# Optimization experiments

Hardware: AMD Instinct MI355X
Metric: run time of the kernel (lower is better)

Reference implementation:

```python
import jax, jax.numpy as jnp
import numpy as np

N = 8192   # number of points (p) == number of reference points (r); must match for final bmm
D = 1024   # feature width of the Linear projections


def setup_inputs() -> dict:
    key = jax.random.key(0)
    ks = jax.random.split(key, 8)
    s = 1.0 / np.sqrt(D)
    return {
        "p": jax.random.normal(ks[0], (N, D), dtype=jnp.float32),
        "r": jax.random.normal(ks[1], (N, D), dtype=jnp.float32),
        "Wh": jax.random.uniform(ks[2], (D, D), jnp.float32, -s, s),
        "bh": jax.random.uniform(ks[3], (D,), jnp.float32, -s, s),
        "Wl": jax.random.uniform(ks[4], (D, D), jnp.float32, -s, s),
        "bl": jax.random.uniform(ks[5], (D,), jnp.float32, -s, s),
        "Wg": jax.random.uniform(ks[6], (D, D), jnp.float32, -s, s),
        "bg": jax.random.uniform(ks[7], (D,), jnp.float32, -s, s),
    }


def reference(p, r, Wh, bh, Wl, bl, Wg, bg):
    # Linear projections (torch Linear: x @ W.T + b)
    q = p @ Wh.T + bh          # [N, D]  M_h(p)
    k = r @ Wl.T + bl          # [N, D]  M_l(r)
    v = p @ Wg.T + bg          # [N, D]  M_g(p)
    scores = q @ k.T           # [N, N]  == bmm(q[None], k[None].transpose(1,2))[0]
    # torch softmax dim=1 on [1, N, N] normalizes over the QUERY axis -> axis=0 here
    attn = jax.nn.softmax(scores, axis=0)
    return p + attn @ v        # residual add
```

## Files before the change

kernel.cpp:

```cpp
#include <hip/hip_runtime.h>
#include <hip/hip_fp16.h>

typedef _Float16 f16;
typedef __attribute__((ext_vector_type(8))) _Float16 f16x8;
typedef __attribute__((ext_vector_type(4))) float f32x4;

#define NPTS 8192
#define DIM  1024
#define HL2E 0.721347520444482f
#define S2SHIFT 50.0f
#define TBUF (128 * 32)

__device__ __forceinline__ void glds16(const void* g, void* l) {
  __builtin_amdgcn_global_load_lds(
      (const __attribute__((address_space(1))) void*)g,
      (__attribute__((address_space(3))) void*)l, 16, 0, 0);
}


__global__ void cvt_f32_f16(const float* __restrict__ src, f16* __restrict__ dst, int n) {
  int i = (blockIdx.x * 256 + threadIdx.x) * 8;
  if (i >= n) return;
  const float4* s = (const float4*)(src + i);
  float4 a = s[0], b = s[1];
  f16x8 o;
  o[0] = (f16)a.x; o[1] = (f16)a.y; o[2] = (f16)a.z; o[3] = (f16)a.w;
  o[4] = (f16)b.x; o[5] = (f16)b.y; o[6] = (f16)b.z; o[7] = (f16)b.w;
  *(f16x8*)(dst + i) = o;
}

__global__ void zero_f32(float* __restrict__ p, int n) {
  int i = blockIdx.x * 256 + threadIdx.x;
  if (i < n) p[i] = 0.f;
}

__global__ void mk_scales(const float* __restrict__ colsum,
                          f16* __restrict__ ics2, f16* __restrict__ ics4) {
  int j = blockIdx.x * 256 + threadIdx.x;
  float r2 = rsqrtf(fmaxf(colsum[j], 1e-20f));
  ics2[j] = (f16)r2;
  ics4[j] = (f16)sqrtf(r2);
}

__global__ void vscale(f16* __restrict__ vt, const f16* __restrict__ ics2) {
  long i = ((long)blockIdx.x * 256 + threadIdx.x) * 8;
  f16x8 v = *(f16x8*)(vt + i);
  f16x8 s = *(const f16x8*)(ics2 + (i & (NPTS - 1)));
  *(f16x8*)(vt + i) = v * s;
}

__global__ void reduce_out(const float* __restrict__ p,
                           const float* __restrict__ pa,
                           const float* __restrict__ pb,
                           float* __restrict__ out) {
  long i = ((long)blockIdx.x * 256 + threadIdx.x) * 4;
  float4 a = *(const float4*)(p + i);
  float4 b = *(const float4*)(pa + i);
  float4 c = *(const float4*)(pb + i);
  a.x += b.x + c.x; a.y += b.y + c.y; a.z += b.z + c.z; a.w += b.w + c.w;
  *(float4*)(out + i) = a;
}

__global__ __launch_bounds__(256, 2)
void proj_fused(const f16* __restrict__ p_h, const f16* __restrict__ r_h,
                const f16* __restrict__ Wh, const f16* __restrict__ Wl,
                const f16* __restrict__ Wg,
                const float* __restrict__ bh, const float* __restrict__ bl,
                const float* __restrict__ bg,
                f16* __restrict__ q_h, f16* __restrict__ k_h,
                f16* __restrict__ vt_h) {
  __shared__ f16 sA[2 * TBUF];
  __shared__ f16 sB[2 * TBUF];
  const int sub = blockIdx.x >> 9;
  const int bl_ = blockIdx.x & 511;
  const long bi = (long)(bl_ & 63) * 128;
  const long bj = (long)(bl_ >> 6) * 128;
  const f16* A = (sub == 1) ? r_h : p_h;
  const f16* B = (sub == 0) ? Wh : (sub == 1) ? Wl : Wg;
  const float* bias = (sub == 0) ? bh : (sub == 1) ? bl : bg;

  const int t = threadIdx.x;
  const int w = t >> 6, l = t & 63;
  const int wm = (w >> 1) * 64, wn = (w & 1) * 64;
  const int lr = l & 15;
  const int fbase = lr * 32 + (((l >> 4) ^ ((lr >> 1) & 3)) * 8);
  const int grow = w * 16 + (l >> 2);
  const int gcol = ((l & 3) ^ ((l >> 3) & 3)) * 8;
  const f16* gA = A + (bi + grow) * (long)DIM + gcol;
  const f16* gB = B + (bj + grow) * (long)DIM + gcol;
  const int lw0 = (w * 16) * 32, lw1 = (64 + w * 16) * 32;

  glds16(gA, sA + lw0);
  glds16(gA + 64l * DIM, sA + lw1);
  glds16(gB, sB + lw0);
  glds16(gB + 64l * DIM, sB + lw1);
  gA += 32; gB += 32;

  f32x4 acc[4][4] = {};
  const int nk = DIM / 32;
  for (int k = 0; k < nk; k++) {
    const int cur = (k & 1) * TBUF, nxt = TBUF - cur;
    __syncthreads();
    if (k + 1 < nk) {
      glds16(gA, sA + nxt + lw0);
      glds16(gA + 64l * DIM, sA + nxt + lw1);
      glds16(gB, sB + nxt + lw0);
      glds16(gB + 64l * DIM, sB + nxt + lw1);
      gA += 32; gB += 32;
    }
    f16x8 af[4], bf[4];
#pragma unroll
    for (int mt = 0; mt < 4; mt++)
      af[mt] = *(const f16x8*)(sA + cur + (wm + mt * 16) * 32 + fbase);
#pragma unroll
    for (int nt = 0; nt < 4; nt++)
      bf[nt] = *(const f16x8*)(sB + cur + (wn + nt * 16) * 32 + fbase);
#pragma unroll
    for (int mt = 0; mt < 4; mt++)
#pragma unroll
      for (int nt = 0; nt < 4; nt++)
        acc[mt][nt] = __builtin_amdgcn_mfma_f32_16x16x32_f16(af[mt], bf[nt], acc[mt][nt], 0, 0, 0);
  }

  const int rbase = (l >> 4) * 4;
  f16* C = (sub == 0) ? q_h : (sub == 1) ? k_h : vt_h;
#pragma unroll
  for (int nt = 0; nt < 4; nt++) {
    const long col = bj + wn + nt * 16 + lr;
    const float bb = bias[col];
#pragma unroll
    for (int mt = 0; mt < 4; mt++) {
      const long row0 = bi + wm + mt * 16 + rbase;
      if (sub < 2) {
#pragma unroll
        for (int g = 0; g < 4; g++)
          C[(row0 + g) * DIM + col] = (f16)(acc[mt][nt][g] + bb);
      } else {
        union { unsigned long long u; f16 h[4]; } pk;
#pragma unroll
        for (int g = 0; g < 4; g++) pk.h[g] = (f16)(acc[mt][nt][g] + bb);
        *(unsigned long long*)(C + col * (long)NPTS + row0) = pk.u;
      }
    }
  }
}

__global__ __launch_bounds__(512, 2)
void gemm_qk(const f16* __restrict__ A, const f16* __restrict__ B,
             f16* __restrict__ S, float* __restrict__ colsum) {
  __shared__ f16 smem[4 * 16384];
  const int b = blockIdx.x;
  const int sx = b & 7;
  const int j = b >> 3;
  const long bi = (long)(j >> 2) * 256;
  const long bj = (long)(sx * 4 + (j & 3)) * 256;

  const int t = threadIdx.x;
  const int w = t >> 6, l = t & 63;
  const int wm = (w >> 2) * 128, wn = (w & 3) * 64;
  const int lr = l & 15;
  const int fbase = lr * 32 + (((l >> 4) ^ ((lr >> 1) & 3)) * 8);
  const int sro = t >> 2;
  const int scol = ((t & 3) ^ ((t >> 3) & 3)) * 8;
  const f16* gAs = A + (bi + sro) * (long)DIM + scol;
  const f16* gBs = B + (bj + sro) * (long)DIM + scol;
  const int ldst = w * 512;

#pragma unroll
  for (int tl = 0; tl < 3; ++tl) {
    f16* d = smem + tl * 16384;
    glds16(gAs + tl * 32,              d + ldst);
    glds16(gAs + tl * 32 + 128l * DIM, d + 4096 + ldst);
    glds16(gBs + tl * 32,              d + 8192 + ldst);
    glds16(gBs + tl * 32 + 128l * DIM, d + 12288 + ldst);
  }
  asm volatile("s_waitcnt vmcnt(8)" ::: "memory");
  __builtin_amdgcn_s_barrier();
  asm volatile("" ::: "memory");

  f32x4 acc[8][4] = {};
#pragma unroll 4
  for (int kt = 0; kt < 32; ++kt) {
    const f16* sa = smem + (kt & 3) * 16384;
    f16* d = smem + ((kt + 3) & 3) * 16384;
    const int ks = (kt + 3 < 32) ? (kt + 3) : 31;
    const f16* as_ = gAs + ks * 32;
    const f16* bs_ = gBs + ks * 32;
    f16x8 af[4], bf[4];

#pragma unroll
    for (int mt = 0; mt < 4; ++mt)
      af[mt] = *(const f16x8*)(sa + (wm + mt * 16) * 32 + fbase);
#pragma unroll
    for (int nt = 0; nt < 4; ++nt)
      bf[nt] = *(const f16x8*)(sa + 8192 + (wn + nt * 16) * 32 + fbase);
    glds16(as_,              d + ldst);
    glds16(as_ + 128l * DIM, d + 4096 + ldst);
#pragma unroll
    for (int mt = 0; mt < 4; ++mt)
#pragma unroll
      for (int nt = 0; nt < 4; ++nt)
        acc[mt][nt] = __builtin_amdgcn_mfma_f32_16x16x32_f16(af[mt], bf[nt], acc[mt][nt], 0, 0, 0);

#pragma unroll
    for (int mt = 0; mt < 4; ++mt)
      af[mt] = *(const f16x8*)(sa + (wm + 64 + mt * 16) * 32 + fbase);
    glds16(bs_,              d + 8192 + ldst);
    glds16(bs_ + 128l * DIM, d + 12288 + ldst);
#pragma unroll
    for (int mt = 0; mt < 4; ++mt)
#pragma unroll
      for (int nt = 0; nt < 4; ++nt)
        acc[4 + mt][nt] = __builtin_amdgcn_mfma_f32_16x16x32_f16(af[mt], bf[nt], acc[4 + mt][nt], 0, 0, 0);

    asm volatile("s_waitcnt vmcnt(8)" ::: "memory");
    __builtin_amdgcn_s_barrier();
    asm volatile("" ::: "memory");
  }

  const int rbase = (l >> 4) * 4;
  float csum[4] = {0.f, 0.f, 0.f, 0.f};
#pragma unroll
  for (int mt = 0; mt < 8; ++mt) {
#pragma unroll
    for (int g = 0; g < 4; ++g) {
      const long row = bi + wm + mt * 16 + rbase + g;
      f16* Srow = S + row * NPTS + bj + wn + lr;
#pragma unroll
      for (int nt = 0; nt < 4; ++nt) {
        float e = exp2f((acc[mt][nt][g] - S2SHIFT) * HL2E);
        e = fminf(e, 240.f);
        f16 eh = (f16)e;
        Srow[nt * 16] = eh;
        float ef = (float)eh;
        csum[nt] += ef * ef;
      }
    }
  }
#pragma unroll
  for (int nt = 0; nt < 4; ++nt) {
    float cs = csum[nt];
    cs += __shfl_xor(cs, 16);
    cs += __shfl_xor(cs, 32);
    if (l < 16) atomicAdd(colsum + (bj + wn + nt * 16 + lr), cs);
  }
}

__global__ __launch_bounds__(512, 2)
void gemm_pv(const f16* __restrict__ Sm, const f16* __restrict__ vt,
             const f16* __restrict__ ics4,
             float* __restrict__ part0, float* __restrict__ part1) {
  __shared__ f16 smem[4 * 16384];
  const int b = blockIdx.x;
  const int sx = b & 7;
  const int q = b >> 3;
  const int bjidx = q & 3;
  const int pr = (q >> 2) * 8 + sx;
  const int split = pr >> 5;
  const long bi = (long)(pr & 31) * 256;
  const long bj = (long)bjidx * 256;
  const long koff = (long)split * (NPTS / 2);

  const int t = threadIdx.x;
  const int w = t >> 6, l = t & 63;
  const int wm = (w >> 2) * 128, wn = (w & 3) * 64;
  const int lr = l & 15;
  const int fbase = lr * 32 + (((l >> 4) ^ ((lr >> 1) & 3)) * 8);
  const int sro = t >> 2;
  const int scol = ((t & 3) ^ ((t >> 3) & 3)) * 8;
  const f16* gAs = Sm + (bi + sro) * (long)NPTS + koff + scol;
  const f16* gBs = vt + (bj + sro) * (long)NPTS + koff + scol;
  const f16* gic = ics4 + koff + (l >> 4) * 8;
  const int ldst = w * 512;

  const int nk = (NPTS / 2) / 32;

  f16x8 icf[2];
  icf[0] = *(const f16x8*)(gic);
  icf[1] = *(const f16x8*)(gic + 32);
#pragma unroll
  for (int tl = 0; tl < 3; ++tl) {
    f16* d = smem + tl * 16384;
    glds16(gAs + tl * 32,               d + ldst);
    glds16(gAs + tl * 32 + 128l * NPTS, d + 4096 + ldst);
    glds16(gBs + tl * 32,               d + 8192 + ldst);
    glds16(gBs + tl * 32 + 128l * NPTS, d + 12288 + ldst);
  }
  asm volatile("s_waitcnt vmcnt(8)" ::: "memory");
  __builtin_amdgcn_s_barrier();
  asm volatile("" ::: "memory");

  f32x4 acc[8][4] = {};
#pragma unroll 4
  for (int kt = 0; kt < nk; ++kt) {
    const f16* sa = smem + (kt & 3) * 16384;
    f16* d = smem + ((kt + 3) & 3) * 16384;
    const int ks = (kt + 3 < nk) ? (kt + 3) : nk - 1;
    const int ki = (kt + 2 < nk) ? (kt + 2) : nk - 1;
    const f16* as_ = gAs + ks * 32;
    const f16* bs_ = gBs + ks * 32;
    f16x8 af[4], bf[4];

    const f16x8 ic_now = icf[kt & 1];
    icf[kt & 1] = *(const f16x8*)(gic + ki * 32);

#pragma unroll
    for (int mt = 0; mt < 4; ++mt) {
      af[mt] = *(const f16x8*)(sa + (wm + mt * 16) * 32 + fbase);
      af[mt] = af[mt] * ic_now;
      af[mt] = af[mt] * af[mt];
    }
#pragma unroll
    for (int nt = 0; nt < 4; ++nt)
      bf[nt] = *(const f16x8*)(sa + 8192 + (wn + nt * 16) * 32 + fbase);
    glds16(as_,               d + ldst);
    glds16(as_ + 128l * NPTS, d + 4096 + ldst);
#pragma unroll
    for (int mt = 0; mt < 4; ++mt)
#pragma unroll
      for (int nt = 0; nt < 4; ++nt)
        acc[mt][nt] = __builtin_amdgcn_mfma_f32_16x16x32_f16(af[mt], bf[nt], acc[mt][nt], 0, 0, 0);

#pragma unroll
    for (int mt = 0; mt < 4; ++mt) {
      af[mt] = *(const f16x8*)(sa + (wm + 64 + mt * 16) * 32 + fbase);
      af[mt] = af[mt] * ic_now;
      af[mt] = af[mt] * af[mt];
    }
    glds16(bs_,               d + 8192 + ldst);
    glds16(bs_ + 128l * NPTS, d + 12288 + ldst);
#pragma unroll
    for (int mt = 0; mt < 4; ++mt)
#pragma unroll
      for (int nt = 0; nt < 4; ++nt)
        acc[4 + mt][nt] = __builtin_amdgcn_mfma_f32_16x16x32_f16(af[mt], bf[nt], acc[4 + mt][nt], 0, 0, 0);

    asm volatile("s_waitcnt vmcnt(10)" ::: "memory");
    __builtin_amdgcn_s_barrier();
    asm volatile("" ::: "memory");
  }

  float* part = split ? part1 : part0;
  const int rbase = (l >> 4) * 4;
#pragma unroll
  for (int mt = 0; mt < 8; ++mt) {
#pragma unroll
    for (int g = 0; g < 4; ++g) {
      const long row = bi + wm + mt * 16 + rbase + g;
      float* Prow = part + row * DIM + bj + wn + lr;
#pragma unroll
      for (int nt = 0; nt < 4; ++nt)
        Prow[nt * 16] = acc[mt][nt][g];
    }
  }
}

extern "C" void kernel_launch(void* const* d_in, const int* in_sizes, int n_in,
                              void* d_out, int out_size, void* d_ws, size_t ws_size,
                              hipStream_t stream) {
  const float* p  = (const float*)d_in[0];
  const float* r  = (const float*)d_in[1];
  const float* Wh = (const float*)d_in[2];
  const float* bh = (const float*)d_in[3];
  const float* Wl = (const float*)d_in[4];
  const float* bl = (const float*)d_in[5];
  const float* Wg = (const float*)d_in[6];
  const float* bg = (const float*)d_in[7];
  float* out = (float*)d_out;

  char* ws = (char*)d_ws;
  f16* q_h  = (f16*)(ws + (0ull  << 20));
  f16* k_h  = (f16*)(ws + (16ull << 20));
  f16* vt_h = (f16*)(ws + (32ull << 20));
  f16* p_h  = (f16*)(ws + (48ull << 20));
  f16* r_h  = (f16*)(ws + (64ull << 20));
  f16* wh_h = (f16*)(ws + (80ull << 20));
  f16* wl_h = (f16*)(ws + (82ull << 20));
  f16* wg_h = (f16*)(ws + (84ull << 20));
  f16* S    = (f16*)(ws + (96ull << 20));
  float* colsum = (float*)(ws + (224ull << 20));
  f16* ics2 = (f16*)(ws + (225ull << 20));
  f16* ics4 = (f16*)(ws + (226ull << 20));
  float* part0 = (float*)(ws + (0ull  << 20));
  float* part1 = (float*)(ws + (48ull << 20));

  const int nP = NPTS * DIM, nW = DIM * DIM;
  cvt_f32_f16<<<nP / 2048, 256, 0, stream>>>(p,  p_h,  nP);
  cvt_f32_f16<<<nP / 2048, 256, 0, stream>>>(r,  r_h,  nP);
  cvt_f32_f16<<<nW / 2048, 256, 0, stream>>>(Wh, wh_h, nW);
  cvt_f32_f16<<<nW / 2048, 256, 0, stream>>>(Wl, wl_h, nW);
  cvt_f32_f16<<<nW / 2048, 256, 0, stream>>>(Wg, wg_h, nW);
  zero_f32<<<NPTS / 256, 256, 0, stream>>>(colsum, NPTS);

  dim3 blk(256);
  proj_fused<<<1536, blk, 0, stream>>>(p_h, r_h, wh_h, wl_h, wg_h,
                                       bh, bl, bg, q_h, k_h, vt_h);
  gemm_qk<<<1024, dim3(512), 0, stream>>>(q_h, k_h, S, colsum);
  mk_scales<<<NPTS / 256, 256, 0, stream>>>(colsum, ics2, ics4);
  vscale<<<(NPTS / 8) * (DIM / 256), 256, 0, stream>>>(vt_h, ics2);
  gemm_pv<<<256, dim3(512), 0, stream>>>(S, vt_h, ics4, part0, part1);
  reduce_out<<<nP / 1024, 256, 0, stream>>>(p, part0, part1, out);
}
```

Measured before the change: 501.4 us.

## Shrink GEMM tiles to 256x128 with 3-stage LDS ring for higher occupancy

```diff
diff --git a/kernel.cpp b/kernel.cpp
--- a/kernel.cpp
+++ b/kernel.cpp
@@ -9,7 +9,7 @@
 #define DIM  1024
 #define HL2E 0.721347520444482f
 #define S2SHIFT 50.0f
-#define TBUF (128 * 32)
+#define BUF3 12288
 
 __device__ __forceinline__ void glds16(const void* g, void* l) {
   __builtin_amdgcn_global_load_lds(
@@ -61,7 +61,7 @@
   *(float4*)(out + i) = a;
 }
 
-__global__ __launch_bounds__(256, 2)
+__global__ __launch_bounds__(512, 4)
 void proj_fused(const f16* __restrict__ p_h, const f16* __restrict__ r_h,
                 const f16* __restrict__ Wh, const f16* __restrict__ Wl,
                 const f16* __restrict__ Wg,
@@ -69,12 +69,12 @@
                 const float* __restrict__ bg,
                 f16* __restrict__ q_h, f16* __restrict__ k_h,
                 f16* __restrict__ vt_h) {
-  __shared__ f16 sA[2 * TBUF];
-  __shared__ f16 sB[2 * TBUF];
-  const int sub = blockIdx.x >> 9;
-  const int bl_ = blockIdx.x & 511;
-  const long bi = (long)(bl_ & 63) * 128;
-  const long bj = (long)(bl_ >> 6) * 128;
+  __shared__ f16 smem[3 * BUF3];
+  const int b = blockIdx.x;
+  const int sub = b >> 8;
+  const int rest = b & 255;
+  const long bj = (long)(rest & 7) * 128;
+  const long bi = (long)(rest >> 3) * 256;
   const f16* A = (sub == 1) ? r_h : p_h;
   const f16* B = (sub == 0) ? Wh : (sub == 1) ? Wl : Wg;
   const float* bias = (sub == 0) ? bh : (sub == 1) ? bl : bg;
@@ -82,82 +82,6 @@
   const int t = threadIdx.x;
   const int w = t >> 6, l = t & 63;
   const int wm = (w >> 1) * 64, wn = (w & 1) * 64;
-  const int lr = l & 15;
-  const int fbase = lr * 32 + (((l >> 4) ^ ((lr >> 1) & 3)) * 8);
-  const int grow = w * 16 + (l >> 2);
-  const int gcol = ((l & 3) ^ ((l >> 3) & 3)) * 8;
-  const f16* gA = A + (bi + grow) * (long)DIM + gcol;
-  const f16* gB = B + (bj + grow) * (long)DIM + gcol;
-  const int lw0 = (w * 16) * 32, lw1 = (64 + w * 16) * 32;
-
-  glds16(gA, sA + lw0);
-  glds16(gA + 64l * DIM, sA + lw1);
-  glds16(gB, sB + lw0);
-  glds16(gB + 64l * DIM, sB + lw1);
-  gA += 32; gB += 32;
-
-  f32x4 acc[4][4] = {};
-  const int nk = DIM / 32;
-  for (int k = 0; k < nk; k++) {
-    const int cur = (k & 1) * TBUF, nxt = TBUF - cur;
-    __syncthreads();
-    if (k + 1 < nk) {
-      glds16(gA, sA + nxt + lw0);
-      glds16(gA + 64l * DIM, sA + nxt + lw1);
-      glds16(gB, sB + nxt + lw0);
-      glds16(gB + 64l * DIM, sB + nxt + lw1);
-      gA += 32; gB += 32;
-    }
-    f16x8 af[4], bf[4];
-#pragma unroll
-    for (int mt = 0; mt < 4; mt++)
-      af[mt] = *(const f16x8*)(sA + cur + (wm + mt * 16) * 32 + fbase);
-#pragma unroll
-    for (int nt = 0; nt < 4; nt++)
-      bf[nt] = *(const f16x8*)(sB + cur + (wn + nt * 16) * 32 + fbase);
-#pragma unroll
-    for (int mt = 0; mt < 4; mt++)
-#pragma unroll
-      for (int nt = 0; nt < 4; nt++)
-        acc[mt][nt] = __builtin_amdgcn_mfma_f32_16x16x32_f16(af[mt], bf[nt], acc[mt][nt], 0, 0, 0);
-  }
-
-  const int rbase = (l >> 4) * 4;
-  f16* C = (sub == 0) ? q_h : (sub == 1) ? k_h : vt_h;
-#pragma unroll
-  for (int nt = 0; nt < 4; nt++) {
-    const long col = bj + wn + nt * 16 + lr;
-    const float bb = bias[col];
-#pragma unroll
-    for (int mt = 0; mt < 4; mt++) {
-      const long row0 = bi + wm + mt * 16 + rbase;
-      if (sub < 2) {
-#pragma unroll
-        for (int g = 0; g < 4; g++)
-          C[(row0 + g) * DIM + col] = (f16)(acc[mt][nt][g] + bb);
-      } else {
-        union { unsigned long long u; f16 h[4]; } pk;
-#pragma unroll
-        for (int g = 0; g < 4; g++) pk.h[g] = (f16)(acc[mt][nt][g] + bb);
-        *(unsigned long long*)(C + col * (long)NPTS + row0) = pk.u;
-      }
-    }
-  }
-}
-
-__global__ __launch_bounds__(512, 2)
-void gemm_qk(const f16* __restrict__ A, const f16* __restrict__ B,
-             f16* __restrict__ S, float* __restrict__ colsum) {
-  __shared__ f16 smem[4 * 16384];
-  const int b = blockIdx.x;
-  const int sx = b & 7;
-  const int j = b >> 3;
-  const long bi = (long)(j >> 2) * 256;
-  const long bj = (long)(sx * 4 + (j & 3)) * 256;
-
-  const int t = threadIdx.x;
-  const int w = t >> 6, l = t & 63;
-  const int wm = (w >> 2) * 128, wn = (w & 3) * 64;
   const int lr = l & 15;
   const int fbase = lr * 32 + (((l >> 4) ^ ((lr >> 1) & 3)) * 8);
   const int sro = t >> 2;
@@ -167,61 +91,133 @@
   const int ldst = w * 512;
 
 #pragma unroll
-  for (int tl = 0; tl < 3; ++tl) {
-    f16* d = smem + tl * 16384;
+  for (int tl = 0; tl < 2; ++tl) {
+    f16* d = smem + tl * BUF3;
     glds16(gAs + tl * 32,              d + ldst);
     glds16(gAs + tl * 32 + 128l * DIM, d + 4096 + ldst);
     glds16(gBs + tl * 32,              d + 8192 + ldst);
-    glds16(gBs + tl * 32 + 128l * DIM, d + 12288 + ldst);
-  }
-  asm volatile("s_waitcnt vmcnt(8)" ::: "memory");
+  }
+  asm volatile("s_waitcnt vmcnt(3)" ::: "memory");
   __builtin_amdgcn_s_barrier();
   asm volatile("" ::: "memory");
 
-  f32x4 acc[8][4] = {};
-#pragma unroll 4
-  for (int kt = 0; kt < 32; ++kt) {
-    const f16* sa = smem + (kt & 3) * 16384;
-    f16* d = smem + ((kt + 3) & 3) * 16384;
-    const int ks = (kt + 3 < 32) ? (kt + 3) : 31;
-    const f16* as_ = gAs + ks * 32;
-    const f16* bs_ = gBs + ks * 32;
+  f32x4 acc[4][4] = {};
+  const int nk = DIM / 32;
+  int cOff = 0, tOff = 2 * BUF3;
+  for (int kt = 0; kt < nk; ++kt) {
+    const f16* sa = smem + cOff;
+    f16* d = smem + tOff;
+    const int ks = (kt + 2 < nk) ? (kt + 2) : nk - 1;
     f16x8 af[4], bf[4];
-
 #pragma unroll
     for (int mt = 0; mt < 4; ++mt)
       af[mt] = *(const f16x8*)(sa + (wm + mt * 16) * 32 + fbase);
 #pragma unroll
     for (int nt = 0; nt < 4; ++nt)
       bf[nt] = *(const f16x8*)(sa + 8192 + (wn + nt * 16) * 32 + fbase);
-    glds16(as_,              d + ldst);
-    glds16(as_ + 128l * DIM, d + 4096 + ldst);
+    glds16(gAs + ks * 32,              d + ldst);
+    glds16(gAs + ks * 32 + 128l * DIM, d + 4096 + ldst);
+    glds16(gBs + ks * 32,              d + 8192 + ldst);
 #pragma unroll
     for (int mt = 0; mt < 4; ++mt)
 #pragma unroll
       for (int nt = 0; nt < 4; ++nt)
         acc[mt][nt] = __builtin_amdgcn_mfma_f32_16x16x32_f16(af[mt], bf[nt], acc[mt][nt], 0, 0, 0);
-
-#pragma unroll
-    for (int mt = 0; mt < 4; ++mt)
-      af[mt] = *(const f16x8*)(sa + (wm + 64 + mt * 16) * 32 + fbase);
-    glds16(bs_,              d + 8192 + ldst);
-    glds16(bs_ + 128l * DIM, d + 12288 + ldst);
-#pragma unroll
-    for (int mt = 0; mt < 4; ++mt)
-#pragma unroll
-      for (int nt = 0; nt < 4; ++nt)
-        acc[4 + mt][nt] = __builtin_amdgcn_mfma_f32_16x16x32_f16(af[mt], bf[nt], acc[4 + mt][nt], 0, 0, 0);
-
-    asm volatile("s_waitcnt vmcnt(8)" ::: "memory");
+    asm volatile("s_waitcnt vmcnt(3)" ::: "memory");
     __builtin_amdgcn_s_barrier();
     asm volatile("" ::: "memory");
+    cOff += BUF3; if (cOff == 3 * BUF3) cOff = 0;
+    tOff += BUF3; if (tOff == 3 * BUF3) tOff = 0;
+  }
+
+  const int rbase = (l >> 4) * 4;
+  f16* C = (sub == 0) ? q_h : (sub == 1) ? k_h : vt_h;
+#pragma unroll
+  for (int nt = 0; nt < 4; ++nt) {
+    const long col = bj + wn + nt * 16 + lr;
+    const float bb = bias[col];
+#pragma unroll
+    for (int mt = 0; mt < 4; ++mt) {
+      const long row0 = bi + wm + mt * 16 + rbase;
+      if (sub < 2) {
+#pragma unroll
+        for (int g = 0; g < 4; ++g)
+          C[(row0 + g) * DIM + col] = (f16)(acc[mt][nt][g] + bb);
+      } else {
+        union { unsigned long long u; f16 h[4]; } pk;
+#pragma unroll
+        for (int g = 0; g < 4; ++g) pk.h[g] = (f16)(acc[mt][nt][g] + bb);
+        *(unsigned long long*)(C + col * (long)NPTS + row0) = pk.u;
+      }
+    }
+  }
+}
+
+__global__ __launch_bounds__(512, 4)
+void gemm_qk(const f16* __restrict__ A, const f16* __restrict__ B,
+             f16* __restrict__ S, float* __restrict__ colsum) {
+  __shared__ f16 smem[3 * BUF3];
+  const int b = blockIdx.x;
+  const int sx = b & 7;
+  const int j = b >> 3;
+  const long bi = (long)(j >> 3) * 256;
+  const long bj = (long)(sx * 8 + (j & 7)) * 128;
+
+  const int t = threadIdx.x;
+  const int w = t >> 6, l = t & 63;
+  const int wm = (w >> 1) * 64, wn = (w & 1) * 64;
+  const int lr = l & 15;
+  const int fbase = lr * 32 + (((l >> 4) ^ ((lr >> 1) & 3)) * 8);
+  const int sro = t >> 2;
+  const int scol = ((t & 3) ^ ((t >> 3) & 3)) * 8;
+  const f16* gAs = A + (bi + sro) * (long)DIM + scol;
+  const f16* gBs = B + (bj + sro) * (long)DIM + scol;
+  const int ldst = w * 512;
+
+#pragma unroll
+  for (int tl = 0; tl < 2; ++tl) {
+    f16* d = smem + tl * BUF3;
+    glds16(gAs + tl * 32,              d + ldst);
+    glds16(gAs + tl * 32 + 128l * DIM, d + 4096 + ldst);
+    glds16(gBs + tl * 32,              d + 8192 + ldst);
+  }
+  asm volatile("s_waitcnt vmcnt(3)" ::: "memory");
+  __builtin_amdgcn_s_barrier();
+  asm volatile("" ::: "memory");
+
+  f32x4 acc[4][4] = {};
+  const int nk = DIM / 32;
+  int cOff = 0, tOff = 2 * BUF3;
+  for (int kt = 0; kt < nk; ++kt) {
+    const f16* sa = smem + cOff;
+    f16* d = smem + tOff;
+    const int ks = (kt + 2 < nk) ? (kt + 2) : nk - 1;
+    f16x8 af[4], bf[4];
+#pragma unroll
+    for (int mt = 0; mt < 4; ++mt)
+      af[mt] = *(const f16x8*)(sa + (wm + mt * 16) * 32 + fbase);
+#pragma unroll
+    for (int nt = 0; nt < 4; ++nt)
+      bf[nt] = *(const f16x8*)(sa + 8192 + (wn + nt * 16) * 32 + fbase);
+    glds16(gAs + ks * 32,              d + ldst);
+    glds16(gAs + ks * 32 + 128l * DIM, d + 4096 + ldst);
+    glds16(gBs + ks * 32,              d + 8192 + ldst);
+#pragma unroll
+    for (int mt = 0; mt < 4; ++mt)
+#pragma unroll
+      for (int nt = 0; nt < 4; ++nt)
+        acc[mt][nt] = __builtin_amdgcn_mfma_f32_16x16x32_f16(af[mt], bf[nt], acc[mt][nt], 0, 0, 0);
+    asm volatile("s_waitcnt vmcnt(3)" ::: "memory");
+    __builtin_amdgcn_s_barrier();
+    asm volatile("" ::: "memory");
+    cOff += BUF3; if (cOff == 3 * BUF3) cOff = 0;
+    tOff += BUF3; if (tOff == 3 * BUF3) tOff = 0;
   }
 
   const int rbase = (l >> 4) * 4;
   float csum[4] = {0.f, 0.f, 0.f, 0.f};
 #pragma unroll
-  for (int mt = 0; mt < 8; ++mt) {
+  for (int mt = 0; mt < 4; ++mt) {
 #pragma unroll
     for (int g = 0; g < 4; ++g) {
       const long row = bi + wm + mt * 16 + rbase + g;
@@ -246,24 +242,23 @@
   }
 }
 
-__global__ __launch_bounds__(512, 2)
+__global__ __launch_bounds__(512, 4)
 void gemm_pv(const f16* __restrict__ Sm, const f16* __restrict__ vt,
              const f16* __restrict__ ics4,
              float* __restrict__ part0, float* __restrict__ part1) {
-  __shared__ f16 smem[4 * 16384];
+  __shared__ f16 smem[3 * BUF3];
   const int b = blockIdx.x;
   const int sx = b & 7;
   const int q = b >> 3;
-  const int bjidx = q & 3;
-  const int pr = (q >> 2) * 8 + sx;
-  const int split = pr >> 5;
-  const long bi = (long)(pr & 31) * 256;
-  const long bj = (long)bjidx * 256;
+  const int pp = sx * 2 + (q & 1);
+  const long bj = (long)(pp & 7) * 128;
+  const int split = pp >> 3;
+  const long bi = (long)(q >> 1) * 256;
   const long koff = (long)split * (NPTS / 2);
 
   const int t = threadIdx.x;
   const int w = t >> 6, l = t & 63;
-  const int wm = (w >> 2) * 128, wn = (w & 3) * 64;
+  const int wm = (w >> 1) * 64, wn = (w & 1) * 64;
   const int lr = l & 15;
   const int fbase = lr * 32 + (((l >> 4) ^ ((lr >> 1) & 3)) * 8);
   const int sro = t >> 2;
@@ -275,35 +270,29 @@
 
   const int nk = (NPTS / 2) / 32;
 
-  f16x8 icf[2];
-  icf[0] = *(const f16x8*)(gic);
-  icf[1] = *(const f16x8*)(gic + 32);
-#pragma unroll
-  for (int tl = 0; tl < 3; ++tl) {
-    f16* d = smem + tl * 16384;
+  f16x8 ic0 = *(const f16x8*)(gic);
+  f16x8 ic1 = *(const f16x8*)(gic + 32);
+#pragma unroll
+  for (int tl = 0; tl < 2; ++tl) {
+    f16* d = smem + tl * BUF3;
     glds16(gAs + tl * 32,               d + ldst);
     glds16(gAs + tl * 32 + 128l * NPTS, d + 4096 + ldst);
     glds16(gBs + tl * 32,               d + 8192 + ldst);
-    glds16(gBs + tl * 32 + 128l * NPTS, d + 12288 + ldst);
-  }
-  asm volatile("s_waitcnt vmcnt(8)" ::: "memory");
+  }
+  asm volatile("s_waitcnt vmcnt(3)" ::: "memory");
   __builtin_amdgcn_s_barrier();
   asm volatile("" ::: "memory");
 
-  f32x4 acc[8][4] = {};
-#pragma unroll 4
+  f32x4 acc[4][4] = {};
+  int cOff = 0, tOff = 2 * BUF3;
   for (int kt = 0; kt < nk; ++kt) {
-    const f16* sa = smem + (kt & 3) * 16384;
-    f16* d = smem + ((kt + 3) & 3) * 16384;
-    const int ks = (kt + 3 < nk) ? (kt + 3) : nk - 1;
-    const int ki = (kt + 2 < nk) ? (kt + 2) : nk - 1;
-    const f16* as_ = gAs + ks * 32;
-    const f16* bs_ = gBs + ks * 32;
+    const f16* sa = smem + cOff;
+    f16* d = smem + tOff;
+    const int ks = (kt + 2 < nk) ? (kt + 2) : nk - 1;
+    const f16x8 ic_now = ic0;
+    ic0 = ic1;
+    ic1 = *(const f16x8*)(gic + ks * 32);
     f16x8 af[4], bf[4];
-
-    const f16x8 ic_now = icf[kt & 1];
-    icf[kt & 1] = *(const f16x8*)(gic + ki * 32);
-
 #pragma unroll
     for (int mt = 0; mt < 4; ++mt) {
       af[mt] = *(const f16x8*)(sa + (wm + mt * 16) * 32 + fbase);
@@ -313,37 +302,25 @@
 #pragma unroll
     for (int nt = 0; nt < 4; ++nt)
       bf[nt] = *(const f16x8*)(sa + 8192 + (wn + nt * 16) * 32 + fbase);
-    glds16(as_,               d + ldst);
-    glds16(as_ + 128l * NPTS, d + 4096 + ldst);
+    glds16(gAs + ks * 32,               d + ldst);
+    glds16(gAs + ks * 32 + 128l * NPTS, d + 4096 + ldst);
+    glds16(gBs + ks * 32,               d + 8192 + ldst);
 #pragma unroll
     for (int mt = 0; mt < 4; ++mt)
 #pragma unroll
       for (int nt = 0; nt < 4; ++nt)
         acc[mt][nt] = __builtin_amdgcn_mfma_f32_16x16x32_f16(af[mt], bf[nt], acc[mt][nt], 0, 0, 0);
-
-#pragma unroll
-    for (int mt = 0; mt < 4; ++mt) {
-      af[mt] = *(const f16x8*)(sa + (wm + 64 + mt * 16) * 32 + fbase);
-      af[mt] = af[mt] * ic_now;
-      af[mt] = af[mt] * af[mt];
-    }
-    glds16(bs_,               d + 8192 + ldst);
-    glds16(bs_ + 128l * NPTS, d + 12288 + ldst);
-#pragma unroll
-    for (int mt = 0; mt < 4; ++mt)
-#pragma unroll
-      for (int nt = 0; nt < 4; ++nt)
-        acc[4 + mt][nt] = __builtin_amdgcn_mfma_f32_16x16x32_f16(af[mt], bf[nt], acc[4 + mt][nt], 0, 0, 0);
-
-    asm volatile("s_waitcnt vmcnt(10)" ::: "memory");
+    asm volatile("s_waitcnt vmcnt(4)" ::: "memory");
     __builtin_amdgcn_s_barrier();
     asm volatile("" ::: "memory");
+    cOff += BUF3; if (cOff == 3 * BUF3) cOff = 0;
+    tOff += BUF3; if (tOff == 3 * BUF3) tOff = 0;
   }
 
   float* part = split ? part1 : part0;
   const int rbase = (l >> 4) * 4;
 #pragma unroll
-  for (int mt = 0; mt < 8; ++mt) {
+  for (int mt = 0; mt < 4; ++mt) {
 #pragma unroll
     for (int g = 0; g < 4; ++g) {
       const long row = bi + wm + mt * 16 + rbase + g;
@@ -392,12 +369,11 @@
   cvt_f32_f16<<<nW / 2048, 256, 0, stream>>>(Wg, wg_h, nW);
   zero_f32<<<NPTS / 256, 256, 0, stream>>>(colsum, NPTS);
 
-  dim3 blk(256);
-  proj_fused<<<1536, blk, 0, stream>>>(p_h, r_h, wh_h, wl_h, wg_h,
-                                       bh, bl, bg, q_h, k_h, vt_h);
-  gemm_qk<<<1024, dim3(512), 0, stream>>>(q_h, k_h, S, colsum);
+  proj_fused<<<768, dim3(512), 0, stream>>>(p_h, r_h, wh_h, wl_h, wg_h,
+                                            bh, bl, bg, q_h, k_h, vt_h);
+  gemm_qk<<<2048, dim3(512), 0, stream>>>(q_h, k_h, S, colsum);
   mk_scales<<<NPTS / 256, 256, 0, stream>>>(colsum, ics2, ics4);
   vscale<<<(NPTS / 8) * (DIM / 256), 256, 0, stream>>>(vt_h, ics2);
-  gemm_pv<<<256, dim3(512), 0, stream>>>(S, vt_h, ics4, part0, part1);
+  gemm_pv<<<512, dim3(512), 0, stream>>>(S, vt_h, ics4, part0, part1);
   reduce_out<<<nP / 1024, 256, 0, stream>>>(p, part0, part1, out);
 }
```

Result: slower. 527.8 us (+5.3%).

## Prefetch next k-tile LDS fragments into registers in QK and PV GEMM loops

Applied to the files above, without the earlier changes.

```diff
diff --git a/kernel.cpp b/kernel.cpp
--- a/kernel.cpp
+++ b/kernel.cpp
@@ -145,6 +145,40 @@
   }
 }
 
+#define QK_BODY(KT, PA, PB, NA, NB)                                          \
+  {                                                                          \
+    const int kq = (KT);                                                     \
+    const f16* sa = smem + (kq & 3) * 16384;                                 \
+    const int ksn = (kq + 1 < 32) ? (kq + 1) : 31;                           \
+    const f16* sn = smem + (ksn & 3) * 16384;                                \
+    f16* d = smem + ((kq + 3) & 3) * 16384;                                  \
+    const int ks = (kq + 3 < 32) ? (kq + 3) : 31;                            \
+    const f16* as_ = gAs + ks * 32;                                          \
+    const f16* bs_ = gBs + ks * 32;                                          \
+    f16x8 af2[4];                                                            \
+    _Pragma("unroll") for (int mt = 0; mt < 4; ++mt)                         \
+      af2[mt] = *(const f16x8*)(sa + (wm + 64 + mt * 16) * 32 + fbase);      \
+    glds16(as_,              d + ldst);                                      \
+    glds16(as_ + 128l * DIM, d + 4096 + ldst);                               \
+    _Pragma("unroll") for (int mt = 0; mt < 4; ++mt)                         \
+      _Pragma("unroll") for (int nt = 0; nt < 4; ++nt)                       \
+        acc[mt][nt] = __builtin_amdgcn_mfma_f32_16x16x32_f16(                \
+            PA[mt], PB[nt], acc[mt][nt], 0, 0, 0);                           \
+    glds16(bs_,              d + 8192 + ldst);                               \
+    glds16(bs_ + 128l * DIM, d + 12288 + ldst);                              \
+    _Pragma("unroll") for (int mt = 0; mt < 4; ++mt)                         \
+      _Pragma("unroll") for (int nt = 0; nt < 4; ++nt)                       \
+        acc[4 + mt][nt] = __builtin_amdgcn_mfma_f32_16x16x32_f16(            \
+            af2[mt], PB[nt], acc[4 + mt][nt], 0, 0, 0);                      \
+    _Pragma("unroll") for (int mt = 0; mt < 4; ++mt)                         \
+      NA[mt] = *(const f16x8*)(sn + (wm + mt * 16) * 32 + fbase);            \
+    _Pragma("unroll") for (int nt = 0; nt < 4; ++nt)                         \
+      NB[nt] = *(const f16x8*)(sn + 8192 + (wn + nt * 16) * 32 + fbase);     \
+    asm volatile("s_waitcnt vmcnt(4)" ::: "memory");                         \
+    __builtin_amdgcn_s_barrier();                                            \
+    asm volatile("" ::: "memory");                                           \
+  }
+
 __global__ __launch_bounds__(512, 2)
 void gemm_qk(const f16* __restrict__ A, const f16* __restrict__ B,
              f16* __restrict__ S, float* __restrict__ colsum) {
@@ -174,48 +208,22 @@
     glds16(gBs + tl * 32,              d + 8192 + ldst);
     glds16(gBs + tl * 32 + 128l * DIM, d + 12288 + ldst);
   }
-  asm volatile("s_waitcnt vmcnt(8)" ::: "memory");
+  asm volatile("s_waitcnt vmcnt(4)" ::: "memory");
   __builtin_amdgcn_s_barrier();
   asm volatile("" ::: "memory");
 
   f32x4 acc[8][4] = {};
-#pragma unroll 4
-  for (int kt = 0; kt < 32; ++kt) {
-    const f16* sa = smem + (kt & 3) * 16384;
-    f16* d = smem + ((kt + 3) & 3) * 16384;
-    const int ks = (kt + 3 < 32) ? (kt + 3) : 31;
-    const f16* as_ = gAs + ks * 32;
-    const f16* bs_ = gBs + ks * 32;
-    f16x8 af[4], bf[4];
-
-#pragma unroll
-    for (int mt = 0; mt < 4; ++mt)
-      af[mt] = *(const f16x8*)(sa + (wm + mt * 16) * 32 + fbase);
-#pragma unroll
-    for (int nt = 0; nt < 4; ++nt)
-      bf[nt] = *(const f16x8*)(sa + 8192 + (wn + nt * 16) * 32 + fbase);
-    glds16(as_,              d + ldst);
-    glds16(as_ + 128l * DIM, d + 4096 + ldst);
-#pragma unroll
-    for (int mt = 0; mt < 4; ++mt)
-#pragma unroll
-      for (int nt = 0; nt < 4; ++nt)
-        acc[mt][nt] = __builtin_amdgcn_mfma_f32_16x16x32_f16(af[mt], bf[nt], acc[mt][nt], 0, 0, 0);
-
-#pragma unroll
-    for (int mt = 0; mt < 4; ++mt)
-      af[mt] = *(const f16x8*)(sa + (wm + 64 + mt * 16) * 32 + fbase);
-    glds16(bs_,              d + 8192 + ldst);
-    glds16(bs_ + 128l * DIM, d + 12288 + ldst);
-#pragma unroll
-    for (int mt = 0; mt < 4; ++mt)
-#pragma unroll
-      for (int nt = 0; nt < 4; ++nt)
-        acc[4 + mt][nt] = __builtin_amdgcn_mfma_f32_16x16x32_f16(af[mt], bf[nt], acc[4 + mt][nt], 0, 0, 0);
-
-    asm volatile("s_waitcnt vmcnt(8)" ::: "memory");
-    __builtin_amdgcn_s_barrier();
-    asm volatile("" ::: "memory");
+  f16x8 a0[4], b0[4], a1[4], b1[4];
+#pragma unroll
+  for (int mt = 0; mt < 4; ++mt)
+    a0[mt] = *(const f16x8*)(smem + (wm + mt * 16) * 32 + fbase);
+#pragma unroll
+  for (int nt = 0; nt < 4; ++nt)
+    b0[nt] = *(const f16x8*)(smem + 8192 + (wn + nt * 16) * 32 + fbase);
+
+  for (int kt = 0; kt < 32; kt += 2) {
+    QK_BODY(kt,     a0, b0, a1, b1)
+    QK_BODY(kt + 1, a1, b1, a0, b0)
   }
 
   const int rbase = (l >> 4) * 4;
@@ -245,6 +253,49 @@
     if (l < 16) atomicAdd(colsum + (bj + wn + nt * 16 + lr), cs);
   }
 }
+
+#define PV_BODY(KT, PA, PB, NA, NB, ICREG)                                   \
+  {                                                                          \
+    const int kp = (KT);                                                     \
+    const f16* sa = smem + (kp & 3) * 16384;                                 \
+    const int ksn = (kp + 1 < nk) ? (kp + 1) : nk - 1;                       \
+    const f16* sn = smem + (ksn & 3) * 16384;                                \
+    f16* d = smem + ((kp + 3) & 3) * 16384;                                  \
+    const int ks = (kp + 3 < nk) ? (kp + 3) : nk - 1;                        \
+    const int ki = (kp + 2 < nk) ? (kp + 2) : nk - 1;                        \
+    const f16* as_ = gAs + ks * 32;                                          \
+    const f16* bs_ = gBs + ks * 32;                                          \
+    const f16x8 icn = ICREG;                         \
+    ICREG = *(const f16x8*)(gic + ki * 32);       \
+    f16x8 af2[4];                                                            \
+    _Pragma("unroll") for (int mt = 0; mt < 4; ++mt)                         \
+      af2[mt] = *(const f16x8*)(sa + (wm + 64 + mt * 16) * 32 + fbase);      \
+    glds16(as_,               d + ldst);                                     \
+    glds16(as_ + 128l * NPTS, d + 4096 + ldst);                              \
+    _Pragma("unroll") for (int mt = 0; mt < 4; ++mt) {                       \
+      PA[mt] = PA[mt] * icn; PA[mt] = PA[mt] * PA[mt];                       \
+    }                                                                        \
+    _Pragma("unroll") for (int mt = 0; mt < 4; ++mt)                         \
+      _Pragma("unroll") for (int nt = 0; nt < 4; ++nt)                       \
+        acc[mt][nt] = __builtin_amdgcn_mfma_f32_16x16x32_f16(                \
+            PA[mt], PB[nt], acc[mt][nt], 0, 0, 0);                           \
+    glds16(bs_,               d + 8192 + ldst);                              \
+    glds16(bs_ + 128l * NPTS, d + 12288 + ldst);                             \
+    _Pragma("unroll") for (int mt = 0; mt < 4; ++mt) {                       \
+      af2[mt] = af2[mt] * icn; af2[mt] = af2[mt] * af2[mt];                  \
+    }                                                                        \
+    _Pragma("unroll") for (int mt = 0; mt < 4; ++mt)                         \
+      _Pragma("unroll") for (int nt = 0; nt < 4; ++nt)                       \
+        acc[4 + mt][nt] = __builtin_amdgcn_mfma_f32_16x16x32_f16(            \
+            af2[mt], PB[nt], acc[4 + mt][nt], 0, 0, 0);                      \
+    _Pragma("unroll") for (int mt = 0; mt < 4; ++mt)                         \
+      NA[mt] = *(const f16x8*)(sn + (wm + mt * 16) * 32 + fbase);            \
+    _Pragma("unroll") for (int nt = 0; nt < 4; ++nt)                         \
+      NB[nt] = *(const f16x8*)(sn + 8192 + (wn + nt * 16) * 32 + fbase);     \
+    asm volatile("s_waitcnt vmcnt(5)" ::: "memory");                         \
+    __builtin_amdgcn_s_barrier();                                            \
+    asm volatile("" ::: "memory");                                           \
+  }
 
 __global__ __launch_bounds__(512, 2)
 void gemm_pv(const f16* __restrict__ Sm, const f16* __restrict__ vt,
@@ -275,9 +326,8 @@
 
   const int nk = (NPTS / 2) / 32;
 
-  f16x8 icf[2];
-  icf[0] = *(const f16x8*)(gic);
-  icf[1] = *(const f16x8*)(gic + 32);
+  f16x8 ic0 = *(const f16x8*)(gic);
+  f16x8 ic1 = *(const f16x8*)(gic + 32);
 #pragma unroll
   for (int tl = 0; tl < 3; ++tl) {
     f16* d = smem + tl * 16384;
@@ -286,58 +336,22 @@
     glds16(gBs + tl * 32,               d + 8192 + ldst);
     glds16(gBs + tl * 32 + 128l * NPTS, d + 12288 + ldst);
   }
-  asm volatile("s_waitcnt vmcnt(8)" ::: "memory");
+  asm volatile("s_waitcnt vmcnt(4)" ::: "memory");
   __builtin_amdgcn_s_barrier();
   asm volatile("" ::: "memory");
 
   f32x4 acc[8][4] = {};
-#pragma unroll 4
-  for (int kt = 0; kt < nk; ++kt) {
-    const f16* sa = smem + (kt & 3) * 16384;
-    f16* d = smem + ((kt + 3) & 3) * 16384;
-    const int ks = (kt + 3 < nk) ? (kt + 3) : nk - 1;
-    const int ki = (kt + 2 < nk) ? (kt + 2) : nk - 1;
-    const f16* as_ = gAs + ks * 32;
-    const f16* bs_ = gBs + ks * 32;
-    f16x8 af[4], bf[4];
-
-    const f16x8 ic_now = icf[kt & 1];
-    icf[kt & 1] = *(const f16x8*)(gic + ki * 32);
-
-#pragma unroll
-    for (int mt = 0; mt < 4; ++mt) {
-      af[mt] = *(const f16x8*)(sa + (wm + mt * 16) * 32 + fbase);
-      af[mt] = af[mt] * ic_now;
-      af[mt] = af[mt] * af[mt];
-    }
-#pragma unroll
-    for (int nt = 0; nt < 4; ++nt)
-      bf[nt] = *(const f16x8*)(sa + 8192 + (wn + nt * 16) * 32 + fbase);
-    glds16(as_,               d + ldst);
-    glds16(as_ + 128l * NPTS, d + 4096 + ldst);
-#pragma unroll
-    for (int mt = 0; mt < 4; ++mt)
-#pragma unroll
-      for (int nt = 0; nt < 4; ++nt)
-        acc[mt][nt] = __builtin_amdgcn_mfma_f32_16x16x32_f16(af[mt], bf[nt], acc[mt][nt], 0, 0, 0);
-
-#pragma unroll
-    for (int mt = 0; mt < 4; ++mt) {
-      af[mt] = *(const f16x8*)(sa + (wm + 64 + mt * 16) * 32 + fbase);
-      af[mt] = af[mt] * ic_now;
-      af[mt] = af[mt] * af[mt];
-    }
-    glds16(bs_,               d + 8192 + ldst);
-    glds16(bs_ + 128l * NPTS, d + 12288 + ldst);
-#pragma unroll
-    for (int mt = 0; mt < 4; ++mt)
-#pragma unroll
-      for (int nt = 0; nt < 4; ++nt)
-        acc[4 + mt][nt] = __builtin_amdgcn_mfma_f32_16x16x32_f16(af[mt], bf[nt], acc[4 + mt][nt], 0, 0, 0);
-
-    asm volatile("s_waitcnt vmcnt(10)" ::: "memory");
-    __builtin_amdgcn_s_barrier();
-    asm volatile("" ::: "memory");
+  f16x8 a0[4], b0[4], a1[4], b1[4];
+#pragma unroll
+  for (int mt = 0; mt < 4; ++mt)
+    a0[mt] = *(const f16x8*)(smem + (wm + mt * 16) * 32 + fbase);
+#pragma unroll
+  for (int nt = 0; nt < 4; ++nt)
+    b0[nt] = *(const f16x8*)(smem + 8192 + (wn + nt * 16) * 32 + fbase);
+
+  for (int kt = 0; kt < nk; kt += 2) {
+    PV_BODY(kt,     a0, b0, a1, b1, ic0)
+    PV_BODY(kt + 1, a1, b1, a0, b0, ic1)
   }
 
   float* part = split ? part1 : part0;
```

New measurement: 492.8 us. About the same (-1.7%).

## Switch QK and PV GEMMs to double-buffered K=64 stages

Applied to the files above, without the earlier changes.

```diff
diff --git a/kernel.cpp b/kernel.cpp
--- a/kernel.cpp
+++ b/kernel.cpp
@@ -148,7 +148,7 @@
 __global__ __launch_bounds__(512, 2)
 void gemm_qk(const f16* __restrict__ A, const f16* __restrict__ B,
              f16* __restrict__ S, float* __restrict__ colsum) {
-  __shared__ f16 smem[4 * 16384];
+  __shared__ f16 smem[2 * 32768];
   const int b = blockIdx.x;
   const int sx = b & 7;
   const int j = b >> 3;
@@ -167,53 +167,49 @@
   const int ldst = w * 512;
 
 #pragma unroll
-  for (int tl = 0; tl < 3; ++tl) {
-    f16* d = smem + tl * 16384;
-    glds16(gAs + tl * 32,              d + ldst);
-    glds16(gAs + tl * 32 + 128l * DIM, d + 4096 + ldst);
-    glds16(gBs + tl * 32,              d + 8192 + ldst);
-    glds16(gBs + tl * 32 + 128l * DIM, d + 12288 + ldst);
-  }
-  asm volatile("s_waitcnt vmcnt(8)" ::: "memory");
+  for (int s = 0; s < 2; ++s) {
+    glds16(gAs + s * 32,              smem + s * 8192 + ldst);
+    glds16(gAs + s * 32 + 128l * DIM, smem + s * 8192 + 4096 + ldst);
+    glds16(gBs + s * 32,              smem + 16384 + s * 8192 + ldst);
+    glds16(gBs + s * 32 + 128l * DIM, smem + 16384 + s * 8192 + 4096 + ldst);
+  }
+  asm volatile("s_waitcnt vmcnt(0)" ::: "memory");
   __builtin_amdgcn_s_barrier();
   asm volatile("" ::: "memory");
 
   f32x4 acc[8][4] = {};
-#pragma unroll 4
-  for (int kt = 0; kt < 32; ++kt) {
-    const f16* sa = smem + (kt & 3) * 16384;
-    f16* d = smem + ((kt + 3) & 3) * 16384;
-    const int ks = (kt + 3 < 32) ? (kt + 3) : 31;
-    const f16* as_ = gAs + ks * 32;
-    const f16* bs_ = gBs + ks * 32;
-    f16x8 af[4], bf[4];
-
-#pragma unroll
-    for (int mt = 0; mt < 4; ++mt)
-      af[mt] = *(const f16x8*)(sa + (wm + mt * 16) * 32 + fbase);
-#pragma unroll
-    for (int nt = 0; nt < 4; ++nt)
-      bf[nt] = *(const f16x8*)(sa + 8192 + (wn + nt * 16) * 32 + fbase);
-    glds16(as_,              d + ldst);
-    glds16(as_ + 128l * DIM, d + 4096 + ldst);
-#pragma unroll
-    for (int mt = 0; mt < 4; ++mt)
-#pragma unroll
-      for (int nt = 0; nt < 4; ++nt)
-        acc[mt][nt] = __builtin_amdgcn_mfma_f32_16x16x32_f16(af[mt], bf[nt], acc[mt][nt], 0, 0, 0);
-
-#pragma unroll
-    for (int mt = 0; mt < 4; ++mt)
-      af[mt] = *(const f16x8*)(sa + (wm + 64 + mt * 16) * 32 + fbase);
-    glds16(bs_,              d + 8192 + ldst);
-    glds16(bs_ + 128l * DIM, d + 12288 + ldst);
-#pragma unroll
-    for (int mt = 0; mt < 4; ++mt)
-#pragma unroll
-      for (int nt = 0; nt < 4; ++nt)
-        acc[4 + mt][nt] = __builtin_amdgcn_mfma_f32_16x16x32_f16(af[mt], bf[nt], acc[4 + mt][nt], 0, 0, 0);
-
-    asm volatile("s_waitcnt vmcnt(8)" ::: "memory");
+  const int nt = DIM / 64;
+  for (int kt = 0; kt < nt; ++kt) {
+    const f16* sa = smem + (kt & 1) * 32768;
+    f16* d = smem + ((kt + 1) & 1) * 32768;
+    const int ks = (kt + 1 < nt) ? kt + 1 : nt - 1;
+    const f16* as_ = gAs + ks * 64;
+    const f16* bs_ = gBs + ks * 64;
+#pragma unroll
+    for (int s = 0; s < 2; ++s) {
+      glds16(as_ + s * 32,              d + s * 8192 + ldst);
+      glds16(as_ + s * 32 + 128l * DIM, d + s * 8192 + 4096 + ldst);
+      glds16(bs_ + s * 32,              d + 16384 + s * 8192 + ldst);
+      glds16(bs_ + s * 32 + 128l * DIM, d + 16384 + s * 8192 + 4096 + ldst);
+    }
+#pragma unroll
+    for (int s = 0; s < 2; ++s) {
+      const f16* ssa = sa + s * 8192;
+      const f16* ssb = sa + 16384 + s * 8192;
+      f16x8 af[8], bf[4];
+#pragma unroll
+      for (int mt = 0; mt < 8; ++mt)
+        af[mt] = *(const f16x8*)(ssa + (wm + mt * 16) * 32 + fbase);
+#pragma unroll
+      for (int n = 0; n < 4; ++n)
+        bf[n] = *(const f16x8*)(ssb + (wn + n * 16) * 32 + fbase);
+#pragma unroll
+      for (int mt = 0; mt < 8; ++mt)
+#pragma unroll
+        for (int n = 0; n < 4; ++n)
+          acc[mt][n] = __builtin_amdgcn_mfma_f32_16x16x32_f16(af[mt], bf[n], acc[mt][n], 0, 0, 0);
+    }
+    asm volatile("s_waitcnt vmcnt(0)" ::: "memory");
     __builtin_amdgcn_s_barrier();
     asm volatile("" ::: "memory");
   }
@@ -227,22 +223,22 @@
       const long row = bi + wm + mt * 16 + rbase + g;
       f16* Srow = S + row * NPTS + bj + wn + lr;
 #pragma unroll
-      for (int nt = 0; nt < 4; ++nt) {
-        float e = exp2f((acc[mt][nt][g] - S2SHIFT) * HL2E);
+      for (int n = 0; n < 4; ++n) {
+        float e = exp2f((acc[mt][n][g] - S2SHIFT) * HL2E);
         e = fminf(e, 240.f);
         f16 eh = (f16)e;
-        Srow[nt * 16] = eh;
+        Srow[n * 16] = eh;
         float ef = (float)eh;
-        csum[nt] += ef * ef;
+        csum[n] += ef * ef;
       }
     }
   }
 #pragma unroll
-  for (int nt = 0; nt < 4; ++nt) {
-    float cs = csum[nt];
+  for (int n = 0; n < 4; ++n) {
+    float cs = csum[n];
     cs += __shfl_xor(cs, 16);
     cs += __shfl_xor(cs, 32);
-    if (l < 16) atomicAdd(colsum + (bj + wn + nt * 16 + lr), cs);
+    if (l < 16) atomicAdd(colsum + (bj + wn + n * 16 + lr), cs);
   }
 }
 
@@ -250,7 +246,7 @@
 void gemm_pv(const f16* __restrict__ Sm, const f16* __restrict__ vt,
              const f16* __restrict__ ics4,
              float* __restrict__ part0, float* __restrict__ part1) {
-  __shared__ f16 smem[4 * 16384];
+  __shared__ f16 smem[2 * 32768];
   const int b = blockIdx.x;
   const int sx = b & 7;
   const int q = b >> 3;
@@ -273,71 +269,63 @@
   const f16* gic = ics4 + koff + (l >> 4) * 8;
   const int ldst = w * 512;
 
-  const int nk = (NPTS / 2) / 32;
-
-  f16x8 icf[2];
-  icf[0] = *(const f16x8*)(gic);
-  icf[1] = *(const f16x8*)(gic + 32);
-#pragma unroll
-  for (int tl = 0; tl < 3; ++tl) {
-    f16* d = smem + tl * 16384;
-    glds16(gAs + tl * 32,               d + ldst);
-    glds16(gAs + tl * 32 + 128l * NPTS, d + 4096 + ldst);
-    glds16(gBs + tl * 32,               d + 8192 + ldst);
-    glds16(gBs + tl * 32 + 128l * NPTS, d + 12288 + ldst);
-  }
-  asm volatile("s_waitcnt vmcnt(8)" ::: "memory");
+  const int nt = (NPTS / 2) / 64;
+
+  f16x8 icc0 = *(const f16x8*)(gic);
+  f16x8 icc1 = *(const f16x8*)(gic + 32);
+#pragma unroll
+  for (int s = 0; s < 2; ++s) {
+    glds16(gAs + s * 32,               smem + s * 8192 + ldst);
+    glds16(gAs + s * 32 + 128l * NPTS, smem + s * 8192 + 4096 + ldst);
+    glds16(gBs + s * 32,               smem + 16384 + s * 8192 + ldst);
+    glds16(gBs + s * 32 + 128l * NPTS, smem + 16384 + s * 8192 + 4096 + ldst);
+  }
+  asm volatile("s_waitcnt vmcnt(0)" ::: "memory");
   __builtin_amdgcn_s_barrier();
   asm volatile("" ::: "memory");
 
   f32x4 acc[8][4] = {};
-#pragma unroll 4
-  for (int kt = 0; kt < nk; ++kt) {
-    const f16* sa = smem + (kt & 3) * 16384;
-    f16* d = smem + ((kt + 3) & 3) * 16384;
-    const int ks = (kt + 3 < nk) ? (kt + 3) : nk - 1;
-    const int ki = (kt + 2 < nk) ? (kt + 2) : nk - 1;
-    const f16* as_ = gAs + ks * 32;
-    const f16* bs_ = gBs + ks * 32;
-    f16x8 af[4], bf[4];
-
-    const f16x8 ic_now = icf[kt & 1];
-    icf[kt & 1] = *(const f16x8*)(gic + ki * 32);
-
-#pragma unroll
-    for (int mt = 0; mt < 4; ++mt) {
-      af[mt] = *(const f16x8*)(sa + (wm + mt * 16) * 32 + fbase);
-      af[mt] = af[mt] * ic_now;
-      af[mt] = af[mt] * af[mt];
-    }
-#pragma unroll
-    for (int nt = 0; nt < 4; ++nt)
-      bf[nt] = *(const f16x8*)(sa + 8192 + (wn + nt * 16) * 32 + fbase);
-    glds16(as_,               d + ldst);
-    glds16(as_ + 128l * NPTS, d + 4096 + ldst);
-#pragma unroll
-    for (int mt = 0; mt < 4; ++mt)
-#pragma unroll
-      for (int nt = 0; nt < 4; ++nt)
-        acc[mt][nt] = __builtin_amdgcn_mfma_f32_16x16x32_f16(af[mt], bf[nt], acc[mt][nt], 0, 0, 0);
-
-#pragma unroll
-    for (int mt = 0; mt < 4; ++mt) {
-      af[mt] = *(const f16x8*)(sa + (wm + 64 + mt * 16) * 32 + fbase);
-      af[mt] = af[mt] * ic_now;
-      af[mt] = af[mt] * af[mt];
-    }
-    glds16(bs_,               d + 8192 + ldst);
-    glds16(bs_ + 128l * NPTS, d + 12288 + ldst);
-#pragma unroll
-    for (int mt = 0; mt < 4; ++mt)
-#pragma unroll
-      for (int nt = 0; nt < 4; ++nt)
-        acc[4 + mt][nt] = __builtin_amdgcn_mfma_f32_16x16x32_f16(af[mt], bf[nt], acc[4 + mt][nt], 0, 0, 0);
-
-    asm volatile("s_waitcnt vmcnt(10)" ::: "memory");
+  for (int kt = 0; kt < nt; ++kt) {
+    const f16* sa = smem + (kt & 1) * 32768;
+    f16* d = smem + ((kt + 1) & 1) * 32768;
+    const int ks = (kt + 1 < nt) ? kt + 1 : nt - 1;
+    const f16* as_ = gAs + ks * 64;
+    const f16* bs_ = gBs + ks * 64;
+    f16x8 icn0 = *(const f16x8*)(gic + ks * 64);
+    f16x8 icn1 = *(const f16x8*)(gic + ks * 64 + 32);
+#pragma unroll
+    for (int s = 0; s < 2; ++s) {
+      glds16(as_ + s * 32,               d + s * 8192 + ldst);
+      glds16(as_ + s * 32 + 128l * NPTS, d + s * 8192 + 4096 + ldst);
+      glds16(bs_ + s * 32,               d + 16384 + s * 8192 + ldst);
+      glds16(bs_ + s * 32 + 128l * NPTS, d + 16384 + s * 8192 + 4096 + ldst);
+    }
+#pragma unroll
+    for (int s = 0; s < 2; ++s) {
+      const f16x8 icv = s ? icc1 : icc0;
+      const f16* ssa = sa + s * 8192;
+      const f16* ssb = sa + 16384 + s * 8192;
+      f16x8 af[8], bf[4];
+#pragma unroll
+      for (int mt = 0; mt < 8; ++mt) {
+        af[mt] = *(const f16x8*)(ssa + (wm + mt * 16) * 32 + fbase);
+        af[mt] = af[mt] * icv;
+        af[mt] = af[mt] * af[mt];
+      }
+#pragma unroll
+      for (int n = 0; n < 4; ++n)
+        bf[n] = *(const f16x8*)(ssb + (wn + n * 16) * 32 + fbase);
+#pragma unroll
+      for (int mt = 0; mt < 8; ++mt)
+#pragma unroll
+        for (int n = 0; n < 4; ++n)
+          acc[mt][n] = __builtin_amdgcn_mfma_f32_16x16x32_f16(af[mt], bf[n], acc[mt][n], 0, 0, 0);
+    }
+    asm volatile("s_waitcnt vmcnt(0)" ::: "memory");
     __builtin_amdgcn_s_barrier();
     asm volatile("" ::: "memory");
+    icc0 = icn0;
+    icc1 = icn1;
   }
 
   float* part = split ? part1 : part0;
@@ -349,8 +337,8 @@
       const long row = bi + wm + mt * 16 + rbase + g;
       float* Prow = part + row * DIM + bj + wn + lr;
 #pragma unroll
-      for (int nt = 0; nt < 4; ++nt)
-        Prow[nt * 16] = acc[mt][nt][g];
+      for (int n = 0; n < 4; ++n)
+        Prow[n * 16] = acc[mt][n][g];
     }
   }
 }
```

Result: slower. 530.8 us (+5.9%).
